# Performance work log

Measured on AMD Instinct MI355X. Metric: run time of the kernel, lower is better.

The kernel has to match this reference:

```python
import jax, jax.numpy as jnp
import numpy as np

B, N, C_IN, C_OUT, K = 4, 4096, 128, 128, 3
EPS = 1e-06
LAMBDA_MAX = 2.0  # compute_lambda_max=False and lambda_max=None -> 2.0


def setup_inputs() -> dict:
    key = jax.random.key(0)
    k1, k2, k3 = jax.random.split(key, 3)
    x = jax.random.normal(k1, (B, N, C_IN), dtype=jnp.float32)
    adj = jax.random.uniform(k2, (B, N, N), dtype=jnp.float32)
    W = jax.random.normal(k3, (C_OUT, K * C_IN), dtype=jnp.float32) * 0.05
    return {"x": x, "adj": adj, "W": W}


def reference(x, adj, W):
    # degree: sum over dim=1 of adj (matches torch adj.sum(dim=1).unsqueeze(-1))
    degree = jnp.sum(adj, axis=1)[:, :, None]          # [B, N, 1]
    lambda_ratio = 2.0 / (LAMBDA_MAX + EPS)

    def cheb_step(z):
        # lr * D * z - lr * A @ z - z, fused elementwise around one bmm
        return lambda_ratio * (degree * z - jnp.einsum('bnm,bmc->bnc', adj, z)) - z

    Z_list = [x, cheb_step(x)]
    for k in range(2, K):
        Z_list.append(2.0 * cheb_step(Z_list[k - 1]) - Z_list[k - 2])

    Z = jnp.stack(Z_list, axis=1)                      # [B, K, N, C]
    # replicate torch .view(B, N, -1) on contiguous [B, K, N, C]
    Z = Z.reshape(Z.shape[0], Z.shape[2], -1)          # [B, N, K*C]
    out = jnp.einsum('bnf,of->bno', Z, W)              # Linear, no bias
    return out
```

## Files before the change

### kernel.cpp

```cpp
#include <hip/hip_runtime.h>


#define NN 4096
#define CF 128
#define NC (NN * CF)
#define NC3 (3 * NC)
#define LRC 0.9999995f

typedef __attribute__((ext_vector_type(8))) short bf16x8;
typedef __attribute__((ext_vector_type(4))) float f32x4;

__device__ __forceinline__ unsigned short f2b(float f) {
    unsigned u = __float_as_uint(f);
    return (unsigned short)((u + 0x7FFFu + ((u >> 16) & 1u)) >> 16);
}

__global__ __launch_bounds__(256) void degree_kernel(const float* __restrict__ adj,
                                                     float* __restrict__ deg) {
    const int b = blockIdx.z;
    const size_t base = (size_t)b * NN * NN;
    const int n0 = blockIdx.x * 1024;
    const int m0 = blockIdx.y * 256;
    const int t = threadIdx.x;
    float4 s = make_float4(0.f, 0.f, 0.f, 0.f);
    const size_t col = (size_t)(n0 + t * 4);
    for (int m = 0; m < 256; ++m) {
        const float4 v = *(const float4*)&adj[base + (size_t)(m0 + m) * NN + col];
        s.x += v.x; s.y += v.y; s.z += v.z; s.w += v.w;
    }
    float* dp = deg + b * NN + n0 + t * 4;
    atomicAdd(dp + 0, s.x);
    atomicAdd(dp + 1, s.y);
    atomicAdd(dp + 2, s.z);
    atomicAdd(dp + 3, s.w);
}

__global__ __launch_bounds__(256) void prep_cast(const float* __restrict__ adj,
                                                 unsigned short* __restrict__ adjB,
                                                 float* __restrict__ deg) {
    const int b = blockIdx.z;
    const size_t base = (size_t)b * NN * NN;
    const int n0 = blockIdx.x * 1024;
    const int m0 = blockIdx.y * 256;
    const int t = threadIdx.x;
    float4 s = make_float4(0.f, 0.f, 0.f, 0.f);
    const size_t col = (size_t)(n0 + t * 4);
    for (int m = 0; m < 256; ++m) {
        const size_t idx = base + (size_t)(m0 + m) * NN + col;
        const float4 v = *(const float4*)&adj[idx];
        s.x += v.x; s.y += v.y; s.z += v.z; s.w += v.w;
        ushort4 o;
        o.x = f2b(v.x); o.y = f2b(v.y); o.z = f2b(v.z); o.w = f2b(v.w);
        *(ushort4*)&adjB[idx] = o;
    }
    float* dp = deg + b * NN + n0 + t * 4;
    atomicAdd(dp + 0, s.x);
    atomicAdd(dp + 1, s.y);
    atomicAdd(dp + 2, s.z);
    atomicAdd(dp + 3, s.w);
}

__global__ __launch_bounds__(256) void transpose_x(const float* __restrict__ x,
                                                   unsigned short* __restrict__ xTb) {
    __shared__ float tile[64][65];
    const int b = blockIdx.z, m0 = blockIdx.x * 64, n0 = blockIdx.y * 64;
    const int t = threadIdx.x;
    const int c = t & 63, r4 = t >> 6;
    const float* xb = x + (size_t)b * NC;
#pragma unroll
    for (int i = 0; i < 16; ++i) {
        int r = i * 4 + r4;
        tile[r][c] = xb[(size_t)(m0 + r) * CF + n0 + c];
    }
    __syncthreads();
    unsigned short* xo = xTb + (size_t)b * NC + (size_t)n0 * NN + m0;
#pragma unroll
    for (int i = 0; i < 16; ++i) {
        int r = i * 4 + r4;
        xo[(size_t)r * NN + c] = f2b(tile[c][r]);
    }
}

__global__ __launch_bounds__(256) void wt_kernel(const float* __restrict__ W,
                                                 float* __restrict__ Wt) {
    const int idx = blockIdx.x * 256 + threadIdx.x;
    const int o = idx / 384;
    const int f = idx % 384;
    Wt[f * 128 + o] = W[idx];
}

template <int MODE, int STAGE>
__global__ __launch_bounds__(256, 2) void mfma_cheb(
    const void* __restrict__ Aglob,
    const unsigned short* __restrict__ Bt,
    const float* __restrict__ deg,
    const float* __restrict__ x,
    float* __restrict__ Zflat,
    unsigned short* __restrict__ z1Tb)
{
    const int t = threadIdx.x;
    const int wv = t >> 6, lane = t & 63, q = lane >> 4, l16 = lane & 15;
    const int m0 = blockIdx.x * 32;
    const int b = blockIdx.y;

    __shared__ __align__(16) short lds[2][2048];

    const int sr = t >> 3;
    const int sg0 = t & 7;
    const int sg = sg0 ^ (sr & 7);

    const float* apf = nullptr;
    const unsigned short* apb = nullptr;
    if (STAGE == 0)
        apf = (const float*)Aglob + (size_t)b * NN * NN + (size_t)(m0 + sr) * NN + sg * 8;
    else
        apb = (const unsigned short*)Aglob + (size_t)b * NN * NN + (size_t)(m0 + sr) * NN + sg * 8;

    const unsigned short* bp[2];
#pragma unroll
    for (int niw = 0; niw < 2; ++niw) {
        const int n = wv * 32 + niw * 16 + l16;
        bp[niw] = Bt + (size_t)b * NC + (size_t)n * NN + q * 8;
    }

    f32x4 acc[2][2];
#pragma unroll
    for (int i = 0; i < 2; ++i)
#pragma unroll
        for (int j = 0; j < 2; ++j) acc[i][j] = (f32x4)0.f;

    const int ldsw = sr * 64 + sg0 * 8;

    float4 v0, v1; bf16x8 rawb;
    if (STAGE == 0) {
        v0 = *(const float4*)(apf + 0);
        v1 = *(const float4*)(apf + 4);
        union { bf16x8 v; unsigned short u[8]; } tmp;
        tmp.u[0] = f2b(v0.x); tmp.u[1] = f2b(v0.y); tmp.u[2] = f2b(v0.z); tmp.u[3] = f2b(v0.w);
        tmp.u[4] = f2b(v1.x); tmp.u[5] = f2b(v1.y); tmp.u[6] = f2b(v1.z); tmp.u[7] = f2b(v1.w);
        *(bf16x8*)&lds[0][ldsw] = tmp.v;
    } else {
        rawb = *(const bf16x8*)(apb + 0);
        *(bf16x8*)&lds[0][ldsw] = rawb;
    }
    bf16x8 bf_cur[2][2];
#pragma unroll
    for (int niw = 0; niw < 2; ++niw)
#pragma unroll
        for (int kh = 0; kh < 2; ++kh)
            bf_cur[niw][kh] = *(const bf16x8*)(bp[niw] + kh * 32);
    __syncthreads();

    for (int s = 0; s < 64; ++s) {
        const int cur = s & 1;
        const int kn = (s + 1) * 64;
        if (s < 63) {
            if (STAGE == 0) {
                v0 = *(const float4*)(apf + kn);
                v1 = *(const float4*)(apf + kn + 4);
            } else {
                rawb = *(const bf16x8*)(apb + kn);
            }
        }
        bf16x8 bf_nxt[2][2];
        if (s < 63) {
#pragma unroll
            for (int niw = 0; niw < 2; ++niw)
#pragma unroll
                for (int kh = 0; kh < 2; ++kh)
                    bf_nxt[niw][kh] = *(const bf16x8*)(bp[niw] + kn + kh * 32);
        }
        bf16x8 af[2][2];
#pragma unroll
        for (int mi = 0; mi < 2; ++mi) {
            const int mloc = mi * 16 + l16;
#pragma unroll
            for (int kh = 0; kh < 2; ++kh) {
                const int slot = (kh * 4 + q) ^ (l16 & 7);
                af[mi][kh] = *(const bf16x8*)&lds[cur][mloc * 64 + slot * 8];
            }
        }
#pragma unroll
        for (int kh = 0; kh < 2; ++kh)
#pragma unroll
            for (int mi = 0; mi < 2; ++mi)
#pragma unroll
                for (int niw = 0; niw < 2; ++niw)
                    acc[mi][niw] = __builtin_amdgcn_mfma_f32_16x16x32_bf16(
                        af[mi][kh], bf_cur[niw][kh], acc[mi][niw], 0, 0, 0);
        if (s < 63) {
            if (STAGE == 0) {
                union { bf16x8 v; unsigned short u[8]; } tmp;
                tmp.u[0] = f2b(v0.x); tmp.u[1] = f2b(v0.y); tmp.u[2] = f2b(v0.z); tmp.u[3] = f2b(v0.w);
                tmp.u[4] = f2b(v1.x); tmp.u[5] = f2b(v1.y); tmp.u[6] = f2b(v1.z); tmp.u[7] = f2b(v1.w);
                *(bf16x8*)&lds[cur ^ 1][ldsw] = tmp.v;
            } else {
                *(bf16x8*)&lds[cur ^ 1][ldsw] = rawb;
            }
        }
        __syncthreads();
#pragma unroll
        for (int niw = 0; niw < 2; ++niw)
#pragma unroll
            for (int kh = 0; kh < 2; ++kh)
                bf_cur[niw][kh] = bf_nxt[niw][kh];
    }

    const float* xb = x + (size_t)b * NC;
    const float* degb = deg + b * NN;
    float* Zf1 = Zflat + (size_t)b * NC3 + NC;
    float* Zf2 = Zflat + (size_t)b * NC3 + 2 * NC;

#pragma unroll
    for (int mi = 0; mi < 2; ++mi) {
        const int mb = m0 + mi * 16 + q * 4;
        const f32x4 dv = *(const f32x4*)(degb + mb);
#pragma unroll
        for (int niw = 0; niw < 2; ++niw) {
            const int n = wv * 32 + niw * 16 + l16;
            const f32x4 a = acc[mi][niw];
            float xv[4];
#pragma unroll
            for (int r = 0; r < 4; ++r) xv[r] = xb[(size_t)(mb + r) * CF + n];
            if (MODE == 1) {
                float z[4];
#pragma unroll
                for (int r = 0; r < 4; ++r) z[r] = LRC * (dv[r] * xv[r] - a[r]) - xv[r];
#pragma unroll
                for (int r = 0; r < 4; ++r) Zf1[(size_t)(mb + r) * CF + n] = z[r];
                ushort4 o;
                o.x = f2b(z[0]); o.y = f2b(z[1]); o.z = f2b(z[2]); o.w = f2b(z[3]);
                *(ushort4*)&z1Tb[(size_t)b * NC + (size_t)n * NN + mb] = o;
            } else {
                float z1r[4];
#pragma unroll
                for (int r = 0; r < 4; ++r) z1r[r] = Zf1[(size_t)(mb + r) * CF + n];
#pragma unroll
                for (int r = 0; r < 4; ++r) {
                    const float c1 = LRC * (dv[r] * z1r[r] - a[r]) - z1r[r];
                    Zf2[(size_t)(mb + r) * CF + n] = 2.f * c1 - xv[r];
                }
            }
        }
    }
}

__global__ __launch_bounds__(256) void gemm_final(const float* __restrict__ Zflat,
                                                  const float* __restrict__ Wt,
                                                  float* __restrict__ out) {
    const int b = blockIdx.z;
    const float* Ab = Zflat + (size_t)b * NC3;
    float* Cb = out + (size_t)b * NC;

    const int t = threadIdx.x;
    const int tx = t & 15, ty = t >> 4;
    const int m0 = blockIdx.y * 64, n0 = blockIdx.x * 64;

    __shared__ float As[16][68];
    __shared__ float Bs[16][64];

    const int arow = t >> 2;
    const int ak4 = (t & 3) << 2;
    const int bk = t >> 4;
    const int bn4 = (t & 15) << 2;

    float4 acc[4];
    acc[0] = acc[1] = acc[2] = acc[3] = make_float4(0.f, 0.f, 0.f, 0.f);

    const float* aptr = Ab + (size_t)(m0 + arow) * 384 + ak4;
    const float* bptr = Wt + (size_t)bk * 128 + n0 + bn4;

    float4 av = *(const float4*)aptr;
    float4 bv = *(const float4*)bptr;

    for (int k0 = 0; k0 < 384; k0 += 16) {
        __syncthreads();
        As[ak4 + 0][arow] = av.x;
        As[ak4 + 1][arow] = av.y;
        As[ak4 + 2][arow] = av.z;
        As[ak4 + 3][arow] = av.w;
        *(float4*)&Bs[bk][bn4] = bv;
        __syncthreads();
        if (k0 + 16 < 384) {
            av = *(const float4*)(aptr + k0 + 16);
            bv = *(const float4*)(bptr + (size_t)(k0 + 16) * 128);
        }
#pragma unroll
        for (int kk = 0; kk < 16; ++kk) {
            const float4 a = *(const float4*)&As[kk][ty << 2];
            const float4 bb = *(const float4*)&Bs[kk][tx << 2];
            acc[0].x += a.x * bb.x; acc[0].y += a.x * bb.y; acc[0].z += a.x * bb.z; acc[0].w += a.x * bb.w;
            acc[1].x += a.y * bb.x; acc[1].y += a.y * bb.y; acc[1].z += a.y * bb.z; acc[1].w += a.y * bb.w;
            acc[2].x += a.z * bb.x; acc[2].y += a.z * bb.y; acc[2].z += a.z * bb.z; acc[2].w += a.z * bb.w;
            acc[3].x += a.w * bb.x; acc[3].y += a.w * bb.y; acc[3].z += a.w * bb.z; acc[3].w += a.w * bb.w;
        }
    }

    const int ncol = n0 + (tx << 2);
#pragma unroll
    for (int i = 0; i < 4; ++i) {
        const int m = m0 + (ty << 2) + i;
        *(float4*)&Cb[(size_t)m * 128 + ncol] = acc[i];
    }
}

extern "C" void kernel_launch(void* const* d_in, const int* in_sizes, int n_in,
                              void* d_out, int out_size, void* d_ws, size_t ws_size,
                              hipStream_t stream) {
    const float* x   = (const float*)d_in[0];
    const float* adj = (const float*)d_in[1];
    const float* W   = (const float*)d_in[2];
    float* out = (float*)d_out;

    char* ws = (char*)d_ws;
    float* Zflat         = (float*)ws;
    unsigned short* xTb  = (unsigned short*)(ws + 25165824);
    unsigned short* z1Tb = (unsigned short*)(ws + 29360128);
    float* deg           = (float*)(ws + 33554432);
    float* Wt            = (float*)(ws + 33619968);
    unsigned short* adjB = (unsigned short*)(ws + 33816576);
    const bool use_cast = ws_size >= (size_t)33816576 + 134217728ull;

    hipMemsetAsync(deg, 0, 4 * NN * sizeof(float), stream);
    if (use_cast)
        prep_cast<<<dim3(4, 16, 4), 256, 0, stream>>>(adj, adjB, deg);
    else
        degree_kernel<<<dim3(4, 16, 4), 256, 0, stream>>>(adj, deg);

    transpose_x<<<dim3(64, 2, 4), 256, 0, stream>>>(x, xTb);
    wt_kernel<<<192, 256, 0, stream>>>(W, Wt);

    for (int b = 0; b < 4; ++b)
        hipMemcpyAsync(Zflat + (size_t)b * NC3, x + (size_t)b * NC,
                       NC * sizeof(float), hipMemcpyDeviceToDevice, stream);

    if (use_cast) {
        mfma_cheb<1, 1><<<dim3(128, 4), 256, 0, stream>>>(adjB, xTb, deg, x, Zflat, z1Tb);
        mfma_cheb<2, 1><<<dim3(128, 4), 256, 0, stream>>>(adjB, z1Tb, deg, x, Zflat, z1Tb);
    } else {
        mfma_cheb<1, 0><<<dim3(128, 4), 256, 0, stream>>>(adj, xTb, deg, x, Zflat, z1Tb);
        mfma_cheb<2, 0><<<dim3(128, 4), 256, 0, stream>>>(adj, z1Tb, deg, x, Zflat, z1Tb);
    }

    gemm_final<<<dim3(2, 64, 4), 256, 0, stream>>>(Zflat, Wt, out);
}
```

Before: 587.0 us.

## Replace narrow-tile cheb GEMM with 128x128 split-K MFMA plus reduction kernels

```diff
diff --git a/kernel.cpp b/kernel.cpp
--- a/kernel.cpp
+++ b/kernel.cpp
@@ -4,7 +4,6 @@
 #define NN 4096
 #define CF 128
 #define NC (NN * CF)
-#define NC3 (3 * NC)
 #define LRC 0.9999995f
 
 typedef __attribute__((ext_vector_type(8))) short bf16x8;
@@ -13,26 +12,6 @@
 __device__ __forceinline__ unsigned short f2b(float f) {
     unsigned u = __float_as_uint(f);
     return (unsigned short)((u + 0x7FFFu + ((u >> 16) & 1u)) >> 16);
-}
-
-__global__ __launch_bounds__(256) void degree_kernel(const float* __restrict__ adj,
-                                                     float* __restrict__ deg) {
-    const int b = blockIdx.z;
-    const size_t base = (size_t)b * NN * NN;
-    const int n0 = blockIdx.x * 1024;
-    const int m0 = blockIdx.y * 256;
-    const int t = threadIdx.x;
-    float4 s = make_float4(0.f, 0.f, 0.f, 0.f);
-    const size_t col = (size_t)(n0 + t * 4);
-    for (int m = 0; m < 256; ++m) {
-        const float4 v = *(const float4*)&adj[base + (size_t)(m0 + m) * NN + col];
-        s.x += v.x; s.y += v.y; s.z += v.z; s.w += v.w;
-    }
-    float* dp = deg + b * NN + n0 + t * 4;
-    atomicAdd(dp + 0, s.x);
-    atomicAdd(dp + 1, s.y);
-    atomicAdd(dp + 2, s.z);
-    atomicAdd(dp + 3, s.w);
 }
 
 __global__ __launch_bounds__(256) void prep_cast(const float* __restrict__ adj,
@@ -89,206 +68,209 @@
     Wt[f * 128 + o] = W[idx];
 }
 
-template <int MODE, int STAGE>
-__global__ __launch_bounds__(256, 2) void mfma_cheb(
-    const void* __restrict__ Aglob,
+__global__ __launch_bounds__(256, 2) void mfma_part(
+    const unsigned short* __restrict__ adjB,
     const unsigned short* __restrict__ Bt,
-    const float* __restrict__ deg,
-    const float* __restrict__ x,
-    float* __restrict__ Zflat,
-    unsigned short* __restrict__ z1Tb)
+    float* __restrict__ Cpart)
 {
     const int t = threadIdx.x;
-    const int wv = t >> 6, lane = t & 63, q = lane >> 4, l16 = lane & 15;
-    const int m0 = blockIdx.x * 32;
-    const int b = blockIdx.y;
-
-    __shared__ __align__(16) short lds[2][2048];
-
-    const int sr = t >> 3;
-    const int sg0 = t & 7;
-    const int sg = sg0 ^ (sr & 7);
-
-    const float* apf = nullptr;
-    const unsigned short* apb = nullptr;
-    if (STAGE == 0)
-        apf = (const float*)Aglob + (size_t)b * NN * NN + (size_t)(m0 + sr) * NN + sg * 8;
-    else
-        apb = (const unsigned short*)Aglob + (size_t)b * NN * NN + (size_t)(m0 + sr) * NN + sg * 8;
-
-    const unsigned short* bp[2];
-#pragma unroll
-    for (int niw = 0; niw < 2; ++niw) {
-        const int n = wv * 32 + niw * 16 + l16;
-        bp[niw] = Bt + (size_t)b * NC + (size_t)n * NN + q * 8;
-    }
-
-    f32x4 acc[2][2];
-#pragma unroll
-    for (int i = 0; i < 2; ++i)
-#pragma unroll
-        for (int j = 0; j < 2; ++j) acc[i][j] = (f32x4)0.f;
-
-    const int ldsw = sr * 64 + sg0 * 8;
-
-    float4 v0, v1; bf16x8 rawb;
-    if (STAGE == 0) {
-        v0 = *(const float4*)(apf + 0);
-        v1 = *(const float4*)(apf + 4);
-        union { bf16x8 v; unsigned short u[8]; } tmp;
-        tmp.u[0] = f2b(v0.x); tmp.u[1] = f2b(v0.y); tmp.u[2] = f2b(v0.z); tmp.u[3] = f2b(v0.w);
-        tmp.u[4] = f2b(v1.x); tmp.u[5] = f2b(v1.y); tmp.u[6] = f2b(v1.z); tmp.u[7] = f2b(v1.w);
-        *(bf16x8*)&lds[0][ldsw] = tmp.v;
-    } else {
-        rawb = *(const bf16x8*)(apb + 0);
-        *(bf16x8*)&lds[0][ldsw] = rawb;
-    }
-    bf16x8 bf_cur[2][2];
-#pragma unroll
-    for (int niw = 0; niw < 2; ++niw)
-#pragma unroll
-        for (int kh = 0; kh < 2; ++kh)
-            bf_cur[niw][kh] = *(const bf16x8*)(bp[niw] + kh * 32);
+    const int w = t >> 6, lane = t & 63, q = lane >> 4, l16 = lane & 15;
+    const int wm = w & 1, wn = w >> 1;
+    const int m0 = blockIdx.x * 128;
+    const int kc = blockIdx.y;
+    const int b  = blockIdx.z;
+
+    __shared__ __align__(16) short As[8192];
+    __shared__ __align__(16) short Bs[8192];
+
+    const int g  = t & 7;
+    const int r0 = t >> 3;
+
+    const unsigned short* ap = adjB + (size_t)b * NN * NN + (size_t)kc * 1024 + g * 8;
+    const unsigned short* bp = Bt   + (size_t)b * NC      + (size_t)kc * 1024 + g * 8;
+
+    f32x4 acc[4][4];
+#pragma unroll
+    for (int i = 0; i < 4; ++i)
+#pragma unroll
+        for (int j = 0; j < 4; ++j) acc[i][j] = (f32x4)0.f;
+
+    bf16x8 ar[4], br[4];
+#pragma unroll
+    for (int i = 0; i < 4; ++i) {
+        const int r = r0 + i * 32;
+        ar[i] = *(const bf16x8*)(ap + (size_t)(m0 + r) * NN);
+        br[i] = *(const bf16x8*)(bp + (size_t)r * NN);
+    }
+
+    for (int it = 0; it < 16; ++it) {
+        __syncthreads();
+#pragma unroll
+        for (int i = 0; i < 4; ++i) {
+            const int r = r0 + i * 32;
+            const int slot = (g ^ (r & 7)) << 3;
+            *(bf16x8*)&As[r * 64 + slot] = ar[i];
+            *(bf16x8*)&Bs[r * 64 + slot] = br[i];
+        }
+        __syncthreads();
+        if (it < 15) {
+            const int kof = (it + 1) * 64;
+#pragma unroll
+            for (int i = 0; i < 4; ++i) {
+                const int r = r0 + i * 32;
+                ar[i] = *(const bf16x8*)(ap + (size_t)(m0 + r) * NN + kof);
+                br[i] = *(const bf16x8*)(bp + (size_t)r * NN + kof);
+            }
+        }
+#pragma unroll
+        for (int kh = 0; kh < 2; ++kh) {
+            bf16x8 af[4], bf[4];
+#pragma unroll
+            for (int i = 0; i < 4; ++i) {
+                const int ml = wm * 64 + i * 16 + l16;
+                af[i] = *(const bf16x8*)&As[ml * 64 + ((((kh << 2) + q) ^ (ml & 7)) << 3)];
+                const int nl = wn * 64 + i * 16 + l16;
+                bf[i] = *(const bf16x8*)&Bs[nl * 64 + ((((kh << 2) + q) ^ (nl & 7)) << 3)];
+            }
+#pragma unroll
+            for (int i = 0; i < 4; ++i)
+#pragma unroll
+                for (int j = 0; j < 4; ++j)
+                    acc[i][j] = __builtin_amdgcn_mfma_f32_16x16x32_bf16(
+                        af[i], bf[j], acc[i][j], 0, 0, 0);
+        }
+    }
+
+    float* Cb = Cpart + (size_t)(b * 4 + kc) * NC;
+#pragma unroll
+    for (int i = 0; i < 4; ++i) {
+        const int mrow = m0 + wm * 64 + i * 16 + q * 4;
+#pragma unroll
+        for (int j = 0; j < 4; ++j) {
+            const int n = wn * 64 + j * 16 + l16;
+#pragma unroll
+            for (int r = 0; r < 4; ++r)
+                Cb[(size_t)(mrow + r) * CF + n] = acc[i][j][r];
+        }
+    }
+}
+
+__global__ __launch_bounds__(256) void reduce_z1(const float* __restrict__ Cpart,
+                                                 const float* __restrict__ x,
+                                                 const float* __restrict__ deg,
+                                                 float* __restrict__ Zf,
+                                                 unsigned short* __restrict__ z1Tb) {
+    __shared__ unsigned short sh[64][68];
+    const int b = blockIdx.z, m0 = blockIdx.x * 64, n0 = blockIdx.y * 64;
+    const int t = threadIdx.x;
+    const int r0 = (t >> 4) * 4, c0 = (t & 15) * 4;
+    const float* degb = deg + b * NN;
+    const float* xb = x + (size_t)b * NC;
+    float* Zf1 = Zf + (size_t)b * 2 * NC;
+#pragma unroll
+    for (int rr = 0; rr < 4; ++rr) {
+        const int m = m0 + r0 + rr;
+        f32x4 s = (f32x4)0.f;
+#pragma unroll
+        for (int kc = 0; kc < 4; ++kc)
+            s += *(const f32x4*)&Cpart[(size_t)(b * 4 + kc) * NC + (size_t)m * CF + n0 + c0];
+        const f32x4 xv = *(const f32x4*)&xb[(size_t)m * CF + n0 + c0];
+        const float d = degb[m];
+        f32x4 z;
+#pragma unroll
+        for (int cc = 0; cc < 4; ++cc) z[cc] = LRC * (d * xv[cc] - s[cc]) - xv[cc];
+        *(f32x4*)&Zf1[(size_t)m * CF + n0 + c0] = z;
+#pragma unroll
+        for (int cc = 0; cc < 4; ++cc) sh[c0 + cc][r0 + rr] = f2b(z[cc]);
+    }
     __syncthreads();
-
-    for (int s = 0; s < 64; ++s) {
-        const int cur = s & 1;
-        const int kn = (s + 1) * 64;
-        if (s < 63) {
-            if (STAGE == 0) {
-                v0 = *(const float4*)(apf + kn);
-                v1 = *(const float4*)(apf + kn + 4);
-            } else {
-                rawb = *(const bf16x8*)(apb + kn);
-            }
-        }
-        bf16x8 bf_nxt[2][2];
-        if (s < 63) {
-#pragma unroll
-            for (int niw = 0; niw < 2; ++niw)
-#pragma unroll
-                for (int kh = 0; kh < 2; ++kh)
-                    bf_nxt[niw][kh] = *(const bf16x8*)(bp[niw] + kn + kh * 32);
-        }
-        bf16x8 af[2][2];
-#pragma unroll
-        for (int mi = 0; mi < 2; ++mi) {
-            const int mloc = mi * 16 + l16;
-#pragma unroll
-            for (int kh = 0; kh < 2; ++kh) {
-                const int slot = (kh * 4 + q) ^ (l16 & 7);
-                af[mi][kh] = *(const bf16x8*)&lds[cur][mloc * 64 + slot * 8];
-            }
-        }
-#pragma unroll
-        for (int kh = 0; kh < 2; ++kh)
-#pragma unroll
-            for (int mi = 0; mi < 2; ++mi)
-#pragma unroll
-                for (int niw = 0; niw < 2; ++niw)
-                    acc[mi][niw] = __builtin_amdgcn_mfma_f32_16x16x32_bf16(
-                        af[mi][kh], bf_cur[niw][kh], acc[mi][niw], 0, 0, 0);
-        if (s < 63) {
-            if (STAGE == 0) {
-                union { bf16x8 v; unsigned short u[8]; } tmp;
-                tmp.u[0] = f2b(v0.x); tmp.u[1] = f2b(v0.y); tmp.u[2] = f2b(v0.z); tmp.u[3] = f2b(v0.w);
-                tmp.u[4] = f2b(v1.x); tmp.u[5] = f2b(v1.y); tmp.u[6] = f2b(v1.z); tmp.u[7] = f2b(v1.w);
-                *(bf16x8*)&lds[cur ^ 1][ldsw] = tmp.v;
-            } else {
-                *(bf16x8*)&lds[cur ^ 1][ldsw] = rawb;
-            }
-        }
-        __syncthreads();
-#pragma unroll
-        for (int niw = 0; niw < 2; ++niw)
-#pragma unroll
-            for (int kh = 0; kh < 2; ++kh)
-                bf_cur[niw][kh] = bf_nxt[niw][kh];
-    }
-
-    const float* xb = x + (size_t)b * NC;
-    const float* degb = deg + b * NN;
-    float* Zf1 = Zflat + (size_t)b * NC3 + NC;
-    float* Zf2 = Zflat + (size_t)b * NC3 + 2 * NC;
-
-#pragma unroll
-    for (int mi = 0; mi < 2; ++mi) {
-        const int mb = m0 + mi * 16 + q * 4;
-        const f32x4 dv = *(const f32x4*)(degb + mb);
-#pragma unroll
-        for (int niw = 0; niw < 2; ++niw) {
-            const int n = wv * 32 + niw * 16 + l16;
-            const f32x4 a = acc[mi][niw];
-            float xv[4];
-#pragma unroll
-            for (int r = 0; r < 4; ++r) xv[r] = xb[(size_t)(mb + r) * CF + n];
-            if (MODE == 1) {
-                float z[4];
-#pragma unroll
-                for (int r = 0; r < 4; ++r) z[r] = LRC * (dv[r] * xv[r] - a[r]) - xv[r];
-#pragma unroll
-                for (int r = 0; r < 4; ++r) Zf1[(size_t)(mb + r) * CF + n] = z[r];
-                ushort4 o;
-                o.x = f2b(z[0]); o.y = f2b(z[1]); o.z = f2b(z[2]); o.w = f2b(z[3]);
-                *(ushort4*)&z1Tb[(size_t)b * NC + (size_t)n * NN + mb] = o;
-            } else {
-                float z1r[4];
-#pragma unroll
-                for (int r = 0; r < 4; ++r) z1r[r] = Zf1[(size_t)(mb + r) * CF + n];
-#pragma unroll
-                for (int r = 0; r < 4; ++r) {
-                    const float c1 = LRC * (dv[r] * z1r[r] - a[r]) - z1r[r];
-                    Zf2[(size_t)(mb + r) * CF + n] = 2.f * c1 - xv[r];
-                }
-            }
-        }
-    }
-}
-
-__global__ __launch_bounds__(256) void gemm_final(const float* __restrict__ Zflat,
+    unsigned short* zo = z1Tb + (size_t)b * NC + (size_t)n0 * NN + m0;
+    const int nl = t >> 2;
+#pragma unroll
+    for (int i = 0; i < 4; ++i) {
+        const int ml = ((t & 3) + i * 4) * 4;
+        ushort4 v;
+        v.x = sh[nl][ml]; v.y = sh[nl][ml + 1]; v.z = sh[nl][ml + 2]; v.w = sh[nl][ml + 3];
+        *(ushort4*)&zo[(size_t)nl * NN + ml] = v;
+    }
+}
+
+__global__ __launch_bounds__(256) void reduce_z2(const float* __restrict__ Cpart,
+                                                 const float* __restrict__ x,
+                                                 const float* __restrict__ deg,
+                                                 float* __restrict__ Zf) {
+    const size_t gidx = (size_t)blockIdx.x * 256 + threadIdx.x;
+    const int b = (int)(gidx / (NC / 4));
+    const size_t rem = gidx % (NC / 4);
+    const int m = (int)(rem / (CF / 4));
+    const int c0 = (int)(rem % (CF / 4)) * 4;
+    f32x4 s = (f32x4)0.f;
+#pragma unroll
+    for (int kc = 0; kc < 4; ++kc)
+        s += *(const f32x4*)&Cpart[(size_t)(b * 4 + kc) * NC + (size_t)m * CF + c0];
+    const f32x4 xv = *(const f32x4*)&x[(size_t)b * NC + (size_t)m * CF + c0];
+    const f32x4 z1 = *(const f32x4*)&Zf[(size_t)b * 2 * NC + (size_t)m * CF + c0];
+    const float d = deg[b * NN + m];
+    f32x4 z;
+#pragma unroll
+    for (int cc = 0; cc < 4; ++cc)
+        z[cc] = 2.f * (LRC * (d * z1[cc] - s[cc]) - z1[cc]) - xv[cc];
+    *(f32x4*)&Zf[(size_t)b * 2 * NC + NC + (size_t)m * CF + c0] = z;
+}
+
+__global__ __launch_bounds__(256) void gemm_final(const float* __restrict__ x,
+                                                  const float* __restrict__ Zf,
                                                   const float* __restrict__ Wt,
                                                   float* __restrict__ out) {
     const int b = blockIdx.z;
-    const float* Ab = Zflat + (size_t)b * NC3;
     float* Cb = out + (size_t)b * NC;
 
     const int t = threadIdx.x;
     const int tx = t & 15, ty = t >> 4;
     const int m0 = blockIdx.y * 64, n0 = blockIdx.x * 64;
 
-    __shared__ float As[16][68];
-    __shared__ float Bs[16][64];
+    __shared__ float Asm[16][68];
+    __shared__ float Bsm[16][64];
 
     const int arow = t >> 2;
     const int ak4 = (t & 3) << 2;
     const int bk = t >> 4;
     const int bn4 = (t & 15) << 2;
 
+    const float* xb = x + (size_t)b * NC;
+
     float4 acc[4];
     acc[0] = acc[1] = acc[2] = acc[3] = make_float4(0.f, 0.f, 0.f, 0.f);
 
-    const float* aptr = Ab + (size_t)(m0 + arow) * 384 + ak4;
     const float* bptr = Wt + (size_t)bk * 128 + n0 + bn4;
 
-    float4 av = *(const float4*)aptr;
+    auto aload = [&](int k) -> float4 {
+        const unsigned G = (unsigned)(m0 + arow) * 384u + (unsigned)k;
+        const int chunk = (int)(G >> 19);
+        const unsigned rem = G & 524287u;
+        const float* src = (chunk == 0) ? xb : (Zf + (size_t)(b * 2 + (chunk - 1)) * NC);
+        return *(const float4*)&src[rem];
+    };
+
+    float4 av = aload(ak4);
     float4 bv = *(const float4*)bptr;
 
     for (int k0 = 0; k0 < 384; k0 += 16) {
         __syncthreads();
-        As[ak4 + 0][arow] = av.x;
-        As[ak4 + 1][arow] = av.y;
-        As[ak4 + 2][arow] = av.z;
-        As[ak4 + 3][arow] = av.w;
-        *(float4*)&Bs[bk][bn4] = bv;
+        Asm[ak4 + 0][arow] = av.x;
+        Asm[ak4 + 1][arow] = av.y;
+        Asm[ak4 + 2][arow] = av.z;
+        Asm[ak4 + 3][arow] = av.w;
+        *(float4*)&Bsm[bk][bn4] = bv;
         __syncthreads();
         if (k0 + 16 < 384) {
-            av = *(const float4*)(aptr + k0 + 16);
+            av = aload(k0 + 16 + ak4);
             bv = *(const float4*)(bptr + (size_t)(k0 + 16) * 128);
         }
 #pragma unroll
         for (int kk = 0; kk < 16; ++kk) {
-            const float4 a = *(const float4*)&As[kk][ty << 2];
-            const float4 bb = *(const float4*)&Bs[kk][tx << 2];
+            const float4 a = *(const float4*)&Asm[kk][ty << 2];
+            const float4 bb = *(const float4*)&Bsm[kk][tx << 2];
             acc[0].x += a.x * bb.x; acc[0].y += a.x * bb.y; acc[0].z += a.x * bb.z; acc[0].w += a.x * bb.w;
             acc[1].x += a.y * bb.x; acc[1].y += a.y * bb.y; acc[1].z += a.y * bb.z; acc[1].w += a.y * bb.w;
             acc[2].x += a.z * bb.x; acc[2].y += a.z * bb.y; acc[2].z += a.z * bb.z; acc[2].w += a.z * bb.w;
@@ -313,34 +295,24 @@
     float* out = (float*)d_out;
 
     char* ws = (char*)d_ws;
-    float* Zflat         = (float*)ws;
-    unsigned short* xTb  = (unsigned short*)(ws + 25165824);
-    unsigned short* z1Tb = (unsigned short*)(ws + 29360128);
-    float* deg           = (float*)(ws + 33554432);
-    float* Wt            = (float*)(ws + 33619968);
-    unsigned short* adjB = (unsigned short*)(ws + 33816576);
-    const bool use_cast = ws_size >= (size_t)33816576 + 134217728ull;
+    unsigned short* adjB = (unsigned short*)ws;
+    float* Cpart         = (float*)(ws + 134217728u);
+    float* Zf            = (float*)(ws + 167772160u);
+    unsigned short* xTb  = (unsigned short*)(ws + 184549376u);
+    unsigned short* z1Tb = (unsigned short*)(ws + 188743680u);
+    float* deg           = (float*)(ws + 192937984u);
+    float* Wt            = (float*)(ws + 193003520u);
 
     hipMemsetAsync(deg, 0, 4 * NN * sizeof(float), stream);
-    if (use_cast)
-        prep_cast<<<dim3(4, 16, 4), 256, 0, stream>>>(adj, adjB, deg);
-    else
-        degree_kernel<<<dim3(4, 16, 4), 256, 0, stream>>>(adj, deg);
-
+    prep_cast<<<dim3(4, 16, 4), 256, 0, stream>>>(adj, adjB, deg);
     transpose_x<<<dim3(64, 2, 4), 256, 0, stream>>>(x, xTb);
     wt_kernel<<<192, 256, 0, stream>>>(W, Wt);
 
-    for (int b = 0; b < 4; ++b)
-        hipMemcpyAsync(Zflat + (size_t)b * NC3, x + (size_t)b * NC,
-                       NC * sizeof(float), hipMemcpyDeviceToDevice, stream);
-
-    if (use_cast) {
-        mfma_cheb<1, 1><<<dim3(128, 4), 256, 0, stream>>>(adjB, xTb, deg, x, Zflat, z1Tb);
-        mfma_cheb<2, 1><<<dim3(128, 4), 256, 0, stream>>>(adjB, z1Tb, deg, x, Zflat, z1Tb);
-    } else {
-        mfma_cheb<1, 0><<<dim3(128, 4), 256, 0, stream>>>(adj, xTb, deg, x, Zflat, z1Tb);
-        mfma_cheb<2, 0><<<dim3(128, 4), 256, 0, stream>>>(adj, z1Tb, deg, x, Zflat, z1Tb);
-    }
-
-    gemm_final<<<dim3(2, 64, 4), 256, 0, stream>>>(Zflat, Wt, out);
-}
+    mfma_part<<<dim3(32, 4, 4), 256, 0, stream>>>(adjB, xTb, Cpart);
+    reduce_z1<<<dim3(64, 2, 4), 256, 0, stream>>>(Cpart, x, deg, Zf, z1Tb);
+
+    mfma_part<<<dim3(32, 4, 4), 256, 0, stream>>>(adjB, z1Tb, Cpart);
+    reduce_z2<<<2048, 256, 0, stream>>>(Cpart, x, deg, Zf);
+
+    gemm_final<<<dim3(2, 64, 4), 256, 0, stream>>>(x, Zf, Wt, out);
+}
```

Measured after the change: 511.5 us. 12.9% less time.
